# Optimization experiments

Hardware: AMD Instinct MI355X
Metric: run time of the kernel (lower is better)

The kernel has to match this reference:

```python
import jax, jax.numpy as jnp
import numpy as np

SEQ, D_IN, D_OUT = 4096, 1024, 1024


def setup_inputs() -> dict:
    key = jax.random.key(0)
    k_emb, k_q, k_k, k_v = jax.random.split(key, 4)
    # torch Linear stores weight as [out, in]; we keep [in, out] for x @ W
    scale = 1.0 / np.sqrt(D_IN)
    return {
        "embeddings": jax.random.normal(k_emb, (SEQ, D_IN), dtype=jnp.float32),
        "w_query": jax.random.uniform(k_q, (D_IN, D_OUT), dtype=jnp.float32, minval=-scale, maxval=scale),
        "w_key": jax.random.uniform(k_k, (D_IN, D_OUT), dtype=jnp.float32, minval=-scale, maxval=scale),
        "w_value": jax.random.uniform(k_v, (D_IN, D_OUT), dtype=jnp.float32, minval=-scale, maxval=scale),
    }


def reference(embeddings, w_query, w_key, w_value):
    # QKV projections (bias=False)
    q = embeddings @ w_query  # [S, D_out]
    k = embeddings @ w_key    # [S, D_out]
    v = embeddings @ w_value  # [S, D_out]
    inv_sqrt_d = 1.0 / jnp.sqrt(jnp.asarray(k.shape[-1], dtype=q.dtype))
    scores = jnp.einsum("sd,td->st", q, k) * inv_sqrt_d  # [S, S]
    weights = jax.nn.softmax(scores, axis=-1)
    return weights @ v  # [S, D_out]
```

## Files before the change

### kernel.cpp

```cpp
#include <hip/hip_runtime.h>
#include <hip/hip_bf16.h>

typedef unsigned short u16;
typedef __bf16 bf16x8 __attribute__((ext_vector_type(8)));
typedef float f32x4 __attribute__((ext_vector_type(4)));
typedef unsigned short u16x8 __attribute__((ext_vector_type(8)));
typedef unsigned short u16x4 __attribute__((ext_vector_type(4)));

__device__ __forceinline__ float bf2f(u16 u) {
  unsigned x = ((unsigned)u) << 16;
  return __builtin_bit_cast(float, x);
}
__device__ __forceinline__ u16 f2bf(float f) {
  unsigned u = __builtin_bit_cast(unsigned, f);
  u += 0x7fffu + ((u >> 16) & 1u);
  return (u16)(u >> 16);
}

__device__ __forceinline__ void gload16(const u16* g, u16* lds) {
  __builtin_amdgcn_global_load_lds(
      (const __attribute__((address_space(1))) void*)g,
      (__attribute__((address_space(3))) void*)lds,
      16, 0, 0);
}

template <int OUT_MODE, int NX, int BK>
__device__ __forceinline__ void gemm_body(
    const u16* __restrict__ A, int lda,
    const u16* __restrict__ B, int ldb,
    void* __restrict__ C, int ldc, int K, float cscale)
{
  __shared__ __align__(16) u16 As[128 * BK];
  __shared__ __align__(16) u16 Bs[128 * BK];

  constexpr int CPR = BK / 8;
  constexpr int RPG = 512 / BK;
  constexpr int IPW = 32 / RPG;

  const int b = blockIdx.x;
  const int by = (b & 7) + 8 * (b / (8 * NX));
  const int bx = (b >> 3) % NX;
  const int m0 = by * 128, n0 = bx * 128;

  const int t = threadIdx.x;
  const int w = t >> 6, l = t & 63;
  const int srow = l / CPR;
  const int lc = l % CPR;
  const int wm = (w >> 1) * 64, wn = (w & 1) * 64;
  const int fr = l & 15;
  const int q = l >> 4;

  f32x4 acc[4][4] = {};

  for (int kt = 0; kt < K; kt += BK) {
    __syncthreads();
#pragma unroll
    for (int j = 0; j < IPW; ++j) {
      const int rr = RPG * (IPW * w + j);
      const int ga = rr + srow;
      const int sch = ((lc ^ (ga & 7))) * 8;
      gload16(A + (size_t)(m0 + ga) * lda + kt + sch, As + rr * BK);
      gload16(B + (size_t)(n0 + ga) * ldb + kt + sch, Bs + rr * BK);
    }
    __syncthreads();

#pragma unroll
    for (int s = 0; s < BK / 32; ++s) {
      bf16x8 af[4], bfr[4];
#pragma unroll
      for (int i = 0; i < 4; ++i) {
        const int ra = wm + 16 * i + fr;
        const int ma = ra & 7;
        af[i] = *(const bf16x8*)(As + ra * BK + (q ^ (ma & 3)) * 8
                                 + (((s & 1) ^ (ma >> 2)) * 32) + (s >> 1) * 64);
      }
#pragma unroll
      for (int i = 0; i < 4; ++i) {
        const int rb = wn + 16 * i + fr;
        const int mb = rb & 7;
        bfr[i] = *(const bf16x8*)(Bs + rb * BK + (q ^ (mb & 3)) * 8
                                  + (((s & 1) ^ (mb >> 2)) * 32) + (s >> 1) * 64);
      }
#pragma unroll
      for (int i = 0; i < 4; ++i)
#pragma unroll
        for (int jj = 0; jj < 4; ++jj)
          acc[i][jj] = __builtin_amdgcn_mfma_f32_16x16x32_bf16(af[i], bfr[jj], acc[i][jj], 0, 0, 0);
    }
  }

  const int er = q * 4;
  const int ec = l & 15;
#pragma unroll
  for (int i = 0; i < 4; ++i)
#pragma unroll
    for (int jj = 0; jj < 4; ++jj)
#pragma unroll
      for (int r = 0; r < 4; ++r) {
        const size_t idx = (size_t)(m0 + wm + 16 * i + er + r) * ldc + (n0 + wn + 16 * jj + ec);
        if (OUT_MODE == 1) ((u16*)C)[idx] = f2bf(acc[i][jj][r] * cscale);
        else               ((float*)C)[idx] = acc[i][jj][r];
      }
}

__global__ __launch_bounds__(256) void gemm_qkv(const u16* __restrict__ A,
                                                const u16* __restrict__ B,
                                                u16* __restrict__ C) {
  gemm_body<1, 24, 64>(A, 1024, B, 1024, C, 3072, 1024, 1.0f);
}
__global__ __launch_bounds__(256) void gemm_score(const u16* __restrict__ QKV,
                                                  u16* __restrict__ S) {
  gemm_body<1, 32, 64>(QKV, 3072, QKV + 1024, 3072, S, 4096, 1024, 0.03125f);
}
__global__ __launch_bounds__(256) void gemm_pv(const u16* __restrict__ S,
                                               const u16* __restrict__ Vt,
                                               float* __restrict__ O) {
  gemm_body<0, 8, 128>(S, 4096, Vt, 4096, O, 1024, 4096, 1.0f);
}

__global__ __launch_bounds__(256) void prep(
    const float* __restrict__ E,
    const float* __restrict__ w0, const float* __restrict__ w1,
    const float* __restrict__ w2,
    u16* __restrict__ Ebf, u16* __restrict__ Wt)
{
  int b = blockIdx.x;
  if (b < 4096) {
    const int i = (b * 256 + threadIdx.x) * 4;
    float4 f = *(const float4*)(E + i);
    u16x4 o;
    o.x = f2bf(f.x); o.y = f2bf(f.y); o.z = f2bf(f.z); o.w = f2bf(f.w);
    *(u16x4*)(Ebf + i) = o;
  } else {
    b -= 4096;
    const int which = b >> 10;
    const int tile = b & 1023;
    const float* in = (which == 0) ? w0 : (which == 1) ? w1 : w2;
    u16* o = Wt + (size_t)which * 1024 * 1024;
    const int c0 = (tile & 31) * 32, r0 = (tile >> 5) * 32;
    __shared__ u16 tl[32][33];
    const int tx = threadIdx.x & 31, ty0 = threadIdx.x >> 5;
#pragma unroll
    for (int k = 0; k < 4; ++k) {
      const int ty = ty0 + k * 8;
      tl[ty][tx] = f2bf(in[(size_t)(r0 + ty) * 1024 + c0 + tx]);
    }
    __syncthreads();
#pragma unroll
    for (int k = 0; k < 4; ++k) {
      const int ty = ty0 + k * 8;
      o[(size_t)(c0 + ty) * 1024 + r0 + tx] = tl[tx][ty];
    }
  }
}

__global__ __launch_bounds__(1024) void transpose_bf16(
    const u16* __restrict__ in, int ldin, u16* __restrict__ out, int ldout)
{
  __shared__ u16 tile[32][33];
  const int c0 = blockIdx.x * 32, r0 = blockIdx.y * 32;
  const int tx = threadIdx.x, ty = threadIdx.y;
  tile[ty][tx] = in[(size_t)(r0 + ty) * ldin + c0 + tx];
  __syncthreads();
  out[(size_t)(c0 + ty) * ldout + r0 + tx] = tile[tx][ty];
}

__global__ __launch_bounds__(256) void softmax_rows(u16* __restrict__ S) {
  const int N = 4096;
  u16* p = S + (size_t)blockIdx.x * N;
  const int t = threadIdx.x;
  u16x8 u0 = ((const u16x8*)p)[t * 2];
  u16x8 u1 = ((const u16x8*)p)[t * 2 + 1];
  float v[16];
#pragma unroll
  for (int i = 0; i < 8; ++i) v[i] = bf2f(u0[i]);
#pragma unroll
  for (int i = 0; i < 8; ++i) v[8 + i] = bf2f(u1[i]);

  float m = -1e30f;
#pragma unroll
  for (int i = 0; i < 16; ++i) m = fmaxf(m, v[i]);
#pragma unroll
  for (int off = 32; off; off >>= 1) m = fmaxf(m, __shfl_xor(m, off));
  __shared__ float red[8];
  if ((t & 63) == 0) red[t >> 6] = m;
  __syncthreads();
  m = fmaxf(fmaxf(red[0], red[1]), fmaxf(red[2], red[3]));

  float s = 0.f;
#pragma unroll
  for (int i = 0; i < 16; ++i) { v[i] = __expf(v[i] - m); s += v[i]; }
#pragma unroll
  for (int off = 32; off; off >>= 1) s += __shfl_xor(s, off);
  if ((t & 63) == 0) red[4 + (t >> 6)] = s;
  __syncthreads();
  s = (red[4] + red[5]) + (red[6] + red[7]);
  const float inv = 1.0f / s;

  u16x8 o0, o1;
#pragma unroll
  for (int i = 0; i < 8; ++i) o0[i] = f2bf(v[i] * inv);
#pragma unroll
  for (int i = 0; i < 8; ++i) o1[i] = f2bf(v[8 + i] * inv);
  ((u16x8*)p)[t * 2] = o0;
  ((u16x8*)p)[t * 2 + 1] = o1;
}

extern "C" void kernel_launch(void* const* d_in, const int* in_sizes, int n_in,
                              void* d_out, int out_size, void* d_ws, size_t ws_size,
                              hipStream_t stream) {
  const float* E  = (const float*)d_in[0];
  const float* Wq = (const float*)d_in[1];
  const float* Wk = (const float*)d_in[2];
  const float* Wv = (const float*)d_in[3];
  float* Out = (float*)d_out;

  char* w = (char*)d_ws;
  u16* Ebf = (u16*)(w);
  u16* Wt  = (u16*)(w + (size_t)(8u << 20));
  u16* QKV = (u16*)(w + (size_t)(14u << 20));
  u16* Vt  = (u16*)(w + (size_t)(38u << 20));
  u16* S   = (u16*)(w + (size_t)(46u << 20));

  prep<<<7168, 256, 0, stream>>>(E, Wq, Wk, Wv, Ebf, Wt);

  gemm_qkv<<<768, 256, 0, stream>>>(Ebf, Wt, QKV);

  transpose_bf16<<<dim3(32, 128), dim3(32, 32), 0, stream>>>(QKV + 2048, 3072, Vt, 4096);

  gemm_score<<<1024, 256, 0, stream>>>(QKV, S);

  softmax_rows<<<4096, 256, 0, stream>>>(S);

  gemm_pv<<<256, 256, 0, stream>>>(S, Vt, Out);
}
```

Measured before the change: 241.3 us.

## Split-K the PV GEMM, fuse V transpose into score kernel, simplify LDS swizzle

The PV GEMM launched only 256 blocks, so it is now split along K into two halves over blockIdx.z, with the second half written to a workspace buffer and summed by a new reduce_add kernel. The standalone V transpose is merged into the score GEMM launch as extra blocks, saving one kernel launch and letting the transpose overlap with GEMM tiles. The LDS read swizzle is also simplified to a single XOR index. The cost is an extra fp32 partial buffer written and read back plus an additional launch; the partial buffer reuses the Ebf/Wt workspace region, which is no longer needed by that point.

```diff
diff --git a/kernel.cpp b/kernel.cpp
--- a/kernel.cpp
+++ b/kernel.cpp
@@ -28,18 +28,15 @@
 __device__ __forceinline__ void gemm_body(
     const u16* __restrict__ A, int lda,
     const u16* __restrict__ B, int ldb,
-    void* __restrict__ C, int ldc, int K, float cscale)
+    void* __restrict__ C, int ldc, int kt0, int Kc, float cscale,
+    u16* As, u16* Bs, int bid)
 {
-  __shared__ __align__(16) u16 As[128 * BK];
-  __shared__ __align__(16) u16 Bs[128 * BK];
-
   constexpr int CPR = BK / 8;
   constexpr int RPG = 512 / BK;
   constexpr int IPW = 32 / RPG;
 
-  const int b = blockIdx.x;
-  const int by = (b & 7) + 8 * (b / (8 * NX));
-  const int bx = (b >> 3) % NX;
+  const int by = (bid & 7) + 8 * (bid / (8 * NX));
+  const int bx = (bid >> 3) % NX;
   const int m0 = by * 128, n0 = bx * 128;
 
   const int t = threadIdx.x;
@@ -52,7 +49,8 @@
 
   f32x4 acc[4][4] = {};
 
-  for (int kt = 0; kt < K; kt += BK) {
+  for (int kk = 0; kk < Kc; kk += BK) {
+    const int kt = kt0 + kk;
     __syncthreads();
 #pragma unroll
     for (int j = 0; j < IPW; ++j) {
@@ -66,20 +64,17 @@
 
 #pragma unroll
     for (int s = 0; s < BK / 32; ++s) {
+      const int j = s * 4 + q;
       bf16x8 af[4], bfr[4];
 #pragma unroll
       for (int i = 0; i < 4; ++i) {
         const int ra = wm + 16 * i + fr;
-        const int ma = ra & 7;
-        af[i] = *(const bf16x8*)(As + ra * BK + (q ^ (ma & 3)) * 8
-                                 + (((s & 1) ^ (ma >> 2)) * 32) + (s >> 1) * 64);
+        af[i] = *(const bf16x8*)(As + ra * BK + (j ^ (ra & 7)) * 8);
       }
 #pragma unroll
       for (int i = 0; i < 4; ++i) {
         const int rb = wn + 16 * i + fr;
-        const int mb = rb & 7;
-        bfr[i] = *(const bf16x8*)(Bs + rb * BK + (q ^ (mb & 3)) * 8
-                                  + (((s & 1) ^ (mb >> 2)) * 32) + (s >> 1) * 64);
+        bfr[i] = *(const bf16x8*)(Bs + rb * BK + (j ^ (rb & 7)) * 8);
       }
 #pragma unroll
       for (int i = 0; i < 4; ++i)
@@ -106,16 +101,54 @@
 __global__ __launch_bounds__(256) void gemm_qkv(const u16* __restrict__ A,
                                                 const u16* __restrict__ B,
                                                 u16* __restrict__ C) {
-  gemm_body<1, 24, 64>(A, 1024, B, 1024, C, 3072, 1024, 1.0f);
-}
-__global__ __launch_bounds__(256) void gemm_score(const u16* __restrict__ QKV,
-                                                  u16* __restrict__ S) {
-  gemm_body<1, 32, 64>(QKV, 3072, QKV + 1024, 3072, S, 4096, 1024, 0.03125f);
-}
+  __shared__ __align__(16) u16 As[128 * 64], Bs[128 * 64];
+  gemm_body<1, 24, 64>(A, 1024, B, 1024, C, 3072, 0, 1024, 1.0f, As, Bs, blockIdx.x);
+}
+
+__global__ __launch_bounds__(256) void score_tv(const u16* __restrict__ QKV,
+                                                u16* __restrict__ S,
+                                                u16* __restrict__ Vt) {
+  __shared__ __align__(16) u16 As[128 * 64], Bs[128 * 64];
+  const int b = blockIdx.x;
+  if (b < 1024) {
+    gemm_body<1, 32, 64>(QKV, 3072, QKV + 1024, 3072, S, 4096, 0, 1024,
+                         0.03125f, As, Bs, b);
+  } else {
+    const int v = b - 1024;
+    const int c0 = (v & 31) * 32;
+    const int r0 = (v >> 5) * 32;
+    u16 (*tl)[33] = (u16(*)[33])As;
+    const int tx = threadIdx.x & 31, ty0 = threadIdx.x >> 5;
+    const u16* Vin = QKV + 2048;
+#pragma unroll
+    for (int k = 0; k < 4; ++k) {
+      const int ty = ty0 + k * 8;
+      tl[ty][tx] = Vin[(size_t)(r0 + ty) * 3072 + c0 + tx];
+    }
+    __syncthreads();
+#pragma unroll
+    for (int k = 0; k < 4; ++k) {
+      const int ty = ty0 + k * 8;
+      Vt[(size_t)(c0 + ty) * 4096 + r0 + tx] = tl[tx][ty];
+    }
+  }
+}
+
 __global__ __launch_bounds__(256) void gemm_pv(const u16* __restrict__ S,
                                                const u16* __restrict__ Vt,
-                                               float* __restrict__ O) {
-  gemm_body<0, 8, 128>(S, 4096, Vt, 4096, O, 1024, 4096, 1.0f);
+                                               float* __restrict__ O0,
+                                               float* __restrict__ O1) {
+  __shared__ __align__(16) u16 As[128 * 128], Bs[128 * 128];
+  float* C = blockIdx.z ? O1 : O0;
+  gemm_body<0, 8, 128>(S, 4096, Vt, 4096, C, 1024, blockIdx.z * 2048, 2048,
+                       1.0f, As, Bs, blockIdx.x);
+}
+
+__global__ __launch_bounds__(256) void reduce_add(float4* __restrict__ out,
+                                                  const float4* __restrict__ p) {
+  const int i = blockIdx.x * 256 + threadIdx.x;
+  float4 a = out[i], b = p[i];
+  out[i] = float4{a.x + b.x, a.y + b.y, a.z + b.z, a.w + b.w};
 }
 
 __global__ __launch_bounds__(256) void prep(
@@ -154,17 +187,6 @@
   }
 }
 
-__global__ __launch_bounds__(1024) void transpose_bf16(
-    const u16* __restrict__ in, int ldin, u16* __restrict__ out, int ldout)
-{
-  __shared__ u16 tile[32][33];
-  const int c0 = blockIdx.x * 32, r0 = blockIdx.y * 32;
-  const int tx = threadIdx.x, ty = threadIdx.y;
-  tile[ty][tx] = in[(size_t)(r0 + ty) * ldin + c0 + tx];
-  __syncthreads();
-  out[(size_t)(c0 + ty) * ldout + r0 + tx] = tile[tx][ty];
-}
-
 __global__ __launch_bounds__(256) void softmax_rows(u16* __restrict__ S) {
   const int N = 4096;
   u16* p = S + (size_t)blockIdx.x * N;
@@ -221,16 +243,16 @@
   u16* QKV = (u16*)(w + (size_t)(14u << 20));
   u16* Vt  = (u16*)(w + (size_t)(38u << 20));
   u16* S   = (u16*)(w + (size_t)(46u << 20));
+  float* P1 = (float*)(w);
 
   prep<<<7168, 256, 0, stream>>>(E, Wq, Wk, Wv, Ebf, Wt);
 
   gemm_qkv<<<768, 256, 0, stream>>>(Ebf, Wt, QKV);
 
-  transpose_bf16<<<dim3(32, 128), dim3(32, 32), 0, stream>>>(QKV + 2048, 3072, Vt, 4096);
-
-  gemm_score<<<1024, 256, 0, stream>>>(QKV, S);
+  score_tv<<<5120, 256, 0, stream>>>(QKV, S, Vt);
 
   softmax_rows<<<4096, 256, 0, stream>>>(S);
 
-  gemm_pv<<<256, 256, 0, stream>>>(S, Vt, Out);
-}
+  gemm_pv<<<dim3(256, 1, 2), 256, 0, stream>>>(S, Vt, Out, P1);
+  reduce_add<<<4096, 256, 0, stream>>>((float4*)Out, (const float4*)P1);
+}
```

New measurement: 220.0 us. 8.8% less time.
